# Optimization experiments

Hardware: AMD Instinct MI355X
Metric: run time of the kernel (lower is better)

## Reference

```python
import jax, jax.numpy as jnp
import numpy as np

NUM_CLASSES = 3
POS_T, NEG_T = 0.5, 0.3
RATIO = 3
W_OBJ, W_CLS, W_LOC = 1.0, 1.0, 2.0


def _pairwise_iou(a, b):
    # a: [N,4] anchors, b: [G,4] gt boxes, xyxy
    ix1 = jnp.maximum(a[:, None, 0], b[None, :, 0])
    iy1 = jnp.maximum(a[:, None, 1], b[None, :, 1])
    ix2 = jnp.minimum(a[:, None, 2], b[None, :, 2])
    iy2 = jnp.minimum(a[:, None, 3], b[None, :, 3])
    inter = jnp.clip(ix2 - ix1, 0) * jnp.clip(iy2 - iy1, 0)
    area_a = (a[:, 2] - a[:, 0]) * (a[:, 3] - a[:, 1])
    area_b = (b[:, 2] - b[:, 0]) * (b[:, 3] - b[:, 1])
    union = area_a[:, None] + area_b[None, :] - inter
    return inter / jnp.maximum(union, 1e-9)


def _masked_mean(x, m):
    c = m.sum()
    return jnp.where(c > 0, (x * m).sum() / jnp.maximum(c, 1.0), 0.0)


def _per_image(pred, anc, ax, ay, aw, ah, boxes_gt, labels_gt):
    # pred: [N, 5+nc]; anc: [N,4]; boxes_gt: [G,4]; labels_gt: [G] in 1..nc
    iou = _pairwise_iou(anc, boxes_gt)              # [N, G]
    best = jnp.argmax(iou, axis=1)
    best_iou = jnp.max(iou, axis=1)
    pos = best_iou >= POS_T
    neg = best_iou < NEG_T
    mb = boxes_gt[best]                             # matched boxes [N,4]
    ml = labels_gt[best]                            # matched labels [N]
    obj_logit = pred[:, 4]
    cls_logit = pred[:, 5:]
    obj_t = pos.astype(pred.dtype)
    # BCEWithLogits (numerically stable)
    obj_loss = jnp.maximum(obj_logit, 0) - obj_logit * obj_t + jnp.log1p(jnp.exp(-jnp.abs(obj_logit)))
    # hard negative mining: top-(3*num_pos) detached obj losses among negatives
    num_pos = pos.sum()
    k = jnp.minimum(RATIO * num_pos, neg.sum())
    cand = jnp.where(neg, jax.lax.stop_gradient(obj_loss), -1.0)
    order = jnp.argsort(-cand)
    ranks = jnp.zeros_like(order).at[order].set(jnp.arange(order.shape[0], dtype=order.dtype))
    sel_neg = neg & (ranks < k)
    loss_obj = _masked_mean(obj_loss, (pos | sel_neg).astype(pred.dtype))
    # classification over positives, labels shifted to 0-based
    logp = jax.nn.log_softmax(cls_logit, axis=-1)
    tgt = jnp.clip(ml - 1, 0)
    ce = -jnp.take_along_axis(logp, tgt[:, None], axis=1)[:, 0]
    loss_cls = _masked_mean(ce, pos.astype(pred.dtype))
    # localization over positives: SmoothL1 on encoded offsets
    gx = (mb[:, 0] + mb[:, 2]) * 0.5
    gy = (mb[:, 1] + mb[:, 3]) * 0.5
    gw = jnp.maximum(mb[:, 2] - mb[:, 0], 1e-6)
    gh = jnp.maximum(mb[:, 3] - mb[:, 1], 1e-6)
    loc_tgt = jnp.stack([(gx - ax) / aw, (gy - ay) / ah,
                         jnp.log(gw / aw), jnp.log(gh / ah)], axis=1)
    d = pred[:, :4] - loc_tgt
    ad = jnp.abs(d)
    sl1 = jnp.where(ad < 1.0, 0.5 * d * d, ad - 0.5)  # [N,4]
    pm = pos.astype(pred.dtype)
    cnt = 4.0 * pm.sum()
    loss_loc = jnp.where(cnt > 0, (sl1 * pm[:, None]).sum() / jnp.maximum(cnt, 1.0), 0.0)
    return loss_obj, loss_cls, loss_loc


def _detection_loss(preds, ancs, gt_boxes, gt_labels):
    B = preds[0].shape[0]
    obj_s = 0.0
    cls_s = 0.0
    loc_s = 0.0
    for pred, anc in zip(preds, ancs):
        Bp, C, H, W = pred.shape
        p = jnp.transpose(pred, (0, 2, 3, 1)).reshape(Bp, -1, 5 + NUM_CLASSES)
        ax = (anc[:, 0] + anc[:, 2]) * 0.5
        ay = (anc[:, 1] + anc[:, 3]) * 0.5
        aw = jnp.maximum(anc[:, 2] - anc[:, 0], 1e-6)
        ah = jnp.maximum(anc[:, 3] - anc[:, 1], 1e-6)
        lo, lc, ll = jax.vmap(
            lambda pb, bb, lb: _per_image(pb, anc, ax, ay, aw, ah, bb, lb)
        )(p, gt_boxes, gt_labels)
        obj_s = obj_s + lo.sum()
        cls_s = cls_s + lc.sum()
        loc_s = loc_s + ll.sum()
    obj_m = obj_s / B
    cls_m = cls_s / B
    loc_m = loc_s / B
    total = W_OBJ * obj_m + W_CLS * cls_m + W_LOC * loc_m
    return total, obj_m, cls_m, loc_m


def setup_inputs() -> dict:
    key = jax.random.key(0)
    k = jax.random.split(key, 8)
    B, G, A = 32, 50, 3
    img = 512.0
    scales = [(128, 128), (64, 64), (32, 32)]
    C = A * (5 + NUM_CLASSES)  # 24

    def make_anchors(H, W):
        stride = img / H
        ys, xs = np.meshgrid(np.arange(H), np.arange(W), indexing="ij")
        cx = (xs + 0.5) * stride
        cy = (ys + 0.5) * stride
        per = []
        for s in (1.0, 1.5, 2.0):
            half = s * stride
            per.append(np.stack([cx - half, cy - half, cx + half, cy + half], axis=-1).reshape(-1, 4))
        b = np.stack(per, axis=1).reshape(-1, 4)  # [H*W*A, 4], A innermost
        return jnp.asarray(b, dtype=jnp.float32)

    preds = [jax.random.normal(k[i], (B, C, H, W), dtype=jnp.float32) for i, (H, W) in enumerate(scales)]
    ancs = [make_anchors(H, W) for (H, W) in scales]
    cx = jax.random.uniform(k[3], (B, G)) * 384.0 + 64.0
    cy = jax.random.uniform(k[4], (B, G)) * 384.0 + 64.0
    w = jax.random.uniform(k[5], (B, G)) * 112.0 + 16.0
    h = jax.random.uniform(k[6], (B, G)) * 112.0 + 16.0
    gt_boxes = jnp.stack([cx - w / 2, cy - h / 2, cx + w / 2, cy + h / 2], axis=-1).astype(jnp.float32)
    gt_labels = jax.random.randint(k[7], (B, G), 1, NUM_CLASSES + 1)
    return {"p0": preds[0], "p1": preds[1], "p2": preds[2],
            "a0": ancs[0], "a1": ancs[1], "a2": ancs[2],
            "gt_boxes": gt_boxes, "gt_labels": gt_labels}


def reference(p0, p1, p2, a0, a1, a2, gt_boxes, gt_labels):
    return _detection_loss([p0, p1, p2], [a0, a1, a2], gt_boxes, gt_labels)
```

## Files before the change

kernel.cpp:

```cpp
#include <hip/hip_runtime.h>

#define WS_ACC_POS   0
#define WS_ACC_NEG   96
#define WS_ACC_OBJ   192
#define WS_ACC_CLS   288
#define WS_ACC_LOC   384
#define WS_SENT      480
#define WS_H1        512
#define WS_DONE      (512 + 96*192*2)
#define WS_TOTAL_U32 (WS_DONE + 96)

#define NBINS        192
#define BIN_OFF      872
#define SUM_SCALE    33554432.0f
#define INV_SUM_SCALE (1.0f/33554432.0f)

__device__ __forceinline__ float sl1f(float d){
  float ad = fabsf(d); return ad < 1.f ? 0.5f*d*d : ad - 0.5f;
}
__device__ __forceinline__ unsigned int rec_cnt(unsigned int v){
  return (v >= 0xA0000000u) ? (v - 0xAAAAAAAAu) : v;
}
__device__ __forceinline__ unsigned int ld_u32(unsigned int* p){
  return __hip_atomic_load(p, __ATOMIC_RELAXED, __HIP_MEMORY_SCOPE_AGENT);
}
__device__ __forceinline__ unsigned long long ld_u64(unsigned long long* p){
  return __hip_atomic_load(p, __ATOMIC_RELAXED, __HIP_MEMORY_SCOPE_AGENT);
}
__device__ __forceinline__ float ld_f32(float* p){
  return __hip_atomic_load(p, __ATOMIC_RELAXED, __HIP_MEMORY_SCOPE_AGENT);
}

__global__ __launch_bounds__(256) void k_main(
    const float* __restrict__ p0, const float* __restrict__ p1, const float* __restrict__ p2,
    const float* __restrict__ gtb, const int* __restrict__ gtl,
    unsigned int* __restrict__ ws, float* __restrict__ out)
{
  const int id = blockIdx.x;
  int s, bIm, chunk, H, lw; const float* p;
  if (id < 2048){ s=0; H=128; lw=7; chunk=id>>5;            bIm=id&31;          p=p0; }
  else if (id < 2560){ s=1; H=64; lw=6; chunk=(id-2048)>>5; bIm=(id-2048)&31;   p=p1; }
  else {              s=2; H=32; lw=5; chunk=(id-2560)>>5;  bIm=(id-2560)&31;   p=p2; }
  const int W = H, HW = H*W;
  const float stride = 512.0f/(float)H;
  const int g = s*32 + bIm;
  const int nb = (s==0) ? 64 : (s==1) ? 16 : 4;
  const int tid = threadIdx.x;

  __shared__ float4 sBox[52];
  __shared__ float  sArea[52], sGx[52], sGy[52], sGw[52], sGh[52];
  __shared__ int    sLbl[52];
  __shared__ int    sNk;
  __shared__ unsigned long long sH[NBINS];
  __shared__ float  sRF[3][4];
  __shared__ unsigned int sRU[4];
  __shared__ int    sLast;

  if (tid < 64){
    const int ymin = (chunk*256)>>lw;
    const int rowc = 256>>lw;
    const float by1 = ((float)ymin+0.5f)*stride - 2.0f*stride;
    const float by2 = ((float)(ymin+rowc-1)+0.5f)*stride + 2.0f*stride;
    bool keep=false; float4 gb=make_float4(0,0,0,0); int lbl=0;
    if (tid < 50){
      gb  = *(const float4*)(gtb + ((size_t)bIm*50 + tid)*4);
      lbl = gtl[bIm*50 + tid];
      keep = (fminf(by2, gb.w) - fmaxf(by1, gb.y)) > 0.f;
    }
    unsigned long long m = __ballot(keep);
    if (keep){
      int idx = __popcll(m & ((1ull<<tid)-1ull));
      sBox[idx]=gb;
      sArea[idx]=(gb.z-gb.x)*(gb.w-gb.y);
      sGx[idx]=(gb.x+gb.z)*0.5f;  sGy[idx]=(gb.y+gb.w)*0.5f;
      sGw[idx]=fmaxf(gb.z-gb.x,1e-6f); sGh[idx]=fmaxf(gb.w-gb.y,1e-6f);
      sLbl[idx]=lbl;
    }
    if (tid==0) sNk = __popcll(m);
  }
  if (tid < NBINS) sH[tid]=0ull;
  __syncthreads();

  const int nk = sNk;
  const int hw  = chunk*256 + tid;
  const int hwW = chunk*256 + (tid & ~63);
  const int y = hw>>lw, x = hw&(W-1);
  const float cx = ((float)x+0.5f)*stride, cy = ((float)y+0.5f)*stride;

  const float* pb = p + (size_t)bIm*24*HW + hw;
  float xo[3];
  #pragma unroll
  for (int a=0;a<3;a++) xo[a] = pb[(size_t)(a*8+4)*HW];

  const int wxlo = (W >= 64) ? (hwW & (W-1)) : 0;
  const int wxhi = (W >= 64) ? (wxlo + 63)   : (W-1);
  const int wylo = hwW>>lw, wyhi = (hwW+63)>>lw;
  const float m2 = 2.0f*stride;
  const float wx1 = ((float)wxlo+0.5f)*stride - m2;
  const float wx2 = ((float)wxhi+0.5f)*stride + m2;
  const float wy1 = ((float)wylo+0.5f)*stride - m2;
  const float wy2 = ((float)wyhi+0.5f)*stride + m2;

  float half[3]; half[0]=stride; half[1]=1.5f*stride; half[2]=2.0f*stride;
  float areaA[3], bi[3], bu[3]; int bj[3];
  #pragma unroll
  for (int a=0;a<3;a++){
    const float aw = 2.0f*half[a];
    areaA[a]=aw*aw; bi[a]=0.f; bu[a]=1e-9f; bj[a]=0;
  }
  for (int j=0;j<nk;j++){
    const float4 gb = sBox[j];
    if (gb.x >= wx2 || gb.z <= wx1 || gb.y >= wy2 || gb.w <= wy1) continue;
    const float ar = sArea[j];
    #pragma unroll
    for (int a=0;a<3;a++){
      const float iy1 = fmaxf(cy-half[a], gb.y), iy2 = fminf(cy+half[a], gb.w);
      const float ih  = fmaxf(iy2-iy1, 0.f);
      const float ix1 = fmaxf(cx-half[a], gb.x), ix2 = fminf(cx+half[a], gb.z);
      const float iw  = fmaxf(ix2-ix1, 0.f);
      const float inter = iw*ih;
      const float un = areaA[a] + ar - inter;
      if (inter*bu[a] > bi[a]*un){ bi[a]=inter; bu[a]=un; bj[a]=j; }
    }
  }

  int accPN=0;
  float accObj=0.f, accCls=0.f, accLoc=0.f;
  #pragma unroll
  for (int a=0;a<3;a++){
    const bool pos = bi[a] >= 0.5f*bu[a];
    const bool neg = bi[a] < 0.3f*bu[a];
    if (pos || neg){
      float objl = fmaxf(xo[a],0.f) - (pos ? xo[a] : 0.f)
                 + __logf(1.f + __expf(-fabsf(xo[a])));
      objl = fmaxf(objl, 0.f);
      if (neg){
        accPN += (1<<16);
        const int bin = min(max((int)(__float_as_uint(objl)>>20) - BIN_OFF, 0), NBINS-1);
        const unsigned long long pack =
            (1ull<<48) | (unsigned long long)__float2uint_rn(objl * SUM_SCALE);
        atomicAdd(&sH[bin], pack);
      } else {
        accPN += 1; accObj += objl;
        const int jb = bj[a];
        const float aw = 2.0f*half[a];
        const float c0=pb[(size_t)(a*8+5)*HW], c1=pb[(size_t)(a*8+6)*HW], c2=pb[(size_t)(a*8+7)*HW];
        const float mm = fmaxf(fmaxf(c0,c1),c2);
        const float lse = mm + __logf(__expf(c0-mm)+__expf(c1-mm)+__expf(c2-mm));
        const int t = max(sLbl[jb]-1, 0);
        const float ct = (t==0)?c0 : (t==1)?c1 : c2;
        accCls += lse - ct;
        const float tx = (sGx[jb]-cx)/aw;
        const float ty = (sGy[jb]-cy)/aw;
        const float tw = __logf(sGw[jb]/aw);
        const float th = __logf(sGh[jb]/aw);
        accLoc += sl1f(pb[(size_t)(a*8+0)*HW]-tx) + sl1f(pb[(size_t)(a*8+1)*HW]-ty)
                + sl1f(pb[(size_t)(a*8+2)*HW]-tw) + sl1f(pb[(size_t)(a*8+3)*HW]-th);
      }
    }
  }

  #pragma unroll
  for (int o=32;o;o>>=1){
    accPN  += __shfl_down(accPN,o,64);
    accObj += __shfl_down(accObj,o,64);
    accCls += __shfl_down(accCls,o,64);
    accLoc += __shfl_down(accLoc,o,64);
  }
  if ((tid & 63)==0){
    const int w = tid>>6;
    sRU[w]=(unsigned)accPN;
    sRF[0][w]=accObj; sRF[1][w]=accCls; sRF[2][w]=accLoc;
  }
  __syncthreads();
  if (tid==0){
    float* wf = (float*)ws;
    unsigned t=0; float ob=0,cl=0,lc=0;
    #pragma unroll
    for (int w=0;w<4;w++){ t+=sRU[w]; ob+=sRF[0][w]; cl+=sRF[1][w]; lc+=sRF[2][w]; }
    const unsigned pc = t & 0xFFFFu, nc = t >> 16;
    if (pc) atomicAdd(&ws[WS_ACC_POS+g], pc);
    if (nc) atomicAdd(&ws[WS_ACC_NEG+g], nc);
    if (ob!=0.f) atomicAdd(&wf[WS_ACC_OBJ+g], ob);
    if (cl!=0.f) atomicAdd(&wf[WS_ACC_CLS+g], cl);
    if (lc!=0.f) atomicAdd(&wf[WS_ACC_LOC+g], lc);
  }
  if (tid < NBINS){
    const unsigned long long v = sH[tid];
    if (v){
      unsigned long long* gH = (unsigned long long*)(ws + WS_H1) + (size_t)g*NBINS;
      atomicAdd(&gH[tid], v);
    }
  }

  __syncthreads();
  if (tid==0){
    __threadfence();
    const unsigned old = atomicAdd(&ws[WS_DONE+g], 1u);
    const unsigned b32 =
        (ld_u32(&ws[WS_SENT])==0xAAAAAAAAu) ? 0xAAAAAAAAu : 0u;
    sLast = ((old - b32) == (unsigned)(nb-1)) ? 1 : 0;
  }
  __syncthreads();
  if (!sLast || tid >= 64) return;

  __threadfence();
  const int lane = tid;
  float* wf = (float*)ws;
  const int pos  = (int)rec_cnt(ld_u32(&ws[WS_ACC_POS+g]));
  const int negc = (int)rec_cnt(ld_u32(&ws[WS_ACC_NEG+g]));
  const int k = min(3*pos, negc);
  float selSum = 0.f;

  if (k > 0){
    const unsigned long long base =
        (ld_u32(&ws[WS_SENT])==0xAAAAAAAAu) ? 0xAAAAAAAAAAAAAAAAull : 0ull;
    unsigned long long* gH = (unsigned long long*)(ws + WS_H1) + (size_t)g*NBINS;
    unsigned int c[3]; float sm[3];
    #pragma unroll
    for (int j=0;j<3;j++){
      const unsigned long long d = ld_u64(&gH[lane*3+j]) - base;
      c[j]  = (unsigned int)(d>>48);
      sm[j] = (float)(d & 0xFFFFFFFFFFFFull) * INV_SUM_SCALE;
    }
    const unsigned int c3 = c[0]+c[1]+c[2];
    unsigned int incl = c3;
    #pragma unroll
    for (int off=1; off<64; off<<=1){
      unsigned int yv = __shfl_down(incl, off, 64);
      if (lane+off < 64) incl += yv;
    }
    const unsigned int excl = incl - c3;
    int   tieL = -1, rL = 0; float avgL = 0.f;
    const bool hit = (excl < (unsigned)k) && (incl >= (unsigned)k);
    if (hit){
      unsigned int cum = excl;
      #pragma unroll
      for (int j=2;j>=0;j--){
        const unsigned int cc = c[j];
        if (cum + cc >= (unsigned)k){
          tieL = lane*3+j; rL = (int)((unsigned)k - cum);
          avgL = sm[j]/(float)cc;
          break;
        }
        cum += cc;
      }
    }
    const unsigned long long hm = __ballot(hit);
    const int src = __ffsll(hm) - 1;
    const int   tie = __shfl(tieL, src, 64);
    const int   r   = __shfl(rL,   src, 64);
    const float avg = __shfl(avgL, src, 64);
    float above = 0.f;
    #pragma unroll
    for (int j=0;j<3;j++) if (lane*3+j > tie) above += sm[j];
    #pragma unroll
    for (int o=32;o;o>>=1) above += __shfl_down(above,o,64);
    selSum = above + (float)r * avg;
  }
  if (lane==0){
    const int cObj = pos + k;
    const float ob = ld_f32(&wf[WS_ACC_OBJ+g]);
    const float cl = ld_f32(&wf[WS_ACC_CLS+g]);
    const float lcs= ld_f32(&wf[WS_ACC_LOC+g]);
    const float lo = (cObj>0) ? (ob+selSum)/(float)cObj : 0.f;
    const float lc = (pos>0)  ? cl/(float)pos           : 0.f;
    const float ll = (pos>0)  ? lcs/(float)(4*pos)      : 0.f;
    const float invB = 1.f/32.f;
    atomicAdd(out+0, (lo + lc + 2.f*ll)*invB);
    atomicAdd(out+1, lo*invB);
    atomicAdd(out+2, lc*invB);
    atomicAdd(out+3, ll*invB);
  }
}

extern "C" void kernel_launch(void* const* d_in, const int* in_sizes, int n_in,
                              void* d_out, int out_size, void* d_ws, size_t ws_size,
                              hipStream_t stream){
  if (ws_size < (size_t)WS_TOTAL_U32*4) return;
  const float* p0  = (const float*)d_in[0];
  const float* p1  = (const float*)d_in[1];
  const float* p2  = (const float*)d_in[2];
  const float* gtb = (const float*)d_in[6];
  const int*   gtl = (const int*)d_in[7];
  unsigned int* ws = (unsigned int*)d_ws;
  float* out = (float*)d_out;

  hipLaunchKernelGGL(k_main, dim3(2688), dim3(256), 0, stream,
                     p0,p1,p2,gtb,gtl,ws,out);
}
```

Measured before the change: 146.6 us.

## Replace atomic last-block reduction with per-block slots and second select kernel

Each block of the main kernel now writes its histogram and scalar partial sums into a private workspace slot instead of atomically accumulating into shared per-image counters and electing a last block through a done counter. A new 96-block kernel sums the slots per image and performs the hard-negative selection and final loss reduction. This removes global atomic contention, the sentinel-based workspace handling and the threadfence handshake, at the cost of an extra kernel launch and more workspace traffic (about 4 MB of slot writes and reads).

```diff
diff --git a/kernel.cpp b/kernel.cpp
--- a/kernel.cpp
+++ b/kernel.cpp
@@ -1,15 +1,7 @@
 #include <hip/hip_runtime.h>
 
-#define WS_ACC_POS   0
-#define WS_ACC_NEG   96
-#define WS_ACC_OBJ   192
-#define WS_ACC_CLS   288
-#define WS_ACC_LOC   384
-#define WS_SENT      480
-#define WS_H1        512
-#define WS_DONE      (512 + 96*192*2)
-#define WS_TOTAL_U32 (WS_DONE + 96)
-
+#define SLOT_U64     200
+#define NBLOCKS      2688
 #define NBINS        192
 #define BIN_OFF      872
 #define SUM_SCALE    33554432.0f
@@ -18,23 +10,11 @@
 __device__ __forceinline__ float sl1f(float d){
   float ad = fabsf(d); return ad < 1.f ? 0.5f*d*d : ad - 0.5f;
 }
-__device__ __forceinline__ unsigned int rec_cnt(unsigned int v){
-  return (v >= 0xA0000000u) ? (v - 0xAAAAAAAAu) : v;
-}
-__device__ __forceinline__ unsigned int ld_u32(unsigned int* p){
-  return __hip_atomic_load(p, __ATOMIC_RELAXED, __HIP_MEMORY_SCOPE_AGENT);
-}
-__device__ __forceinline__ unsigned long long ld_u64(unsigned long long* p){
-  return __hip_atomic_load(p, __ATOMIC_RELAXED, __HIP_MEMORY_SCOPE_AGENT);
-}
-__device__ __forceinline__ float ld_f32(float* p){
-  return __hip_atomic_load(p, __ATOMIC_RELAXED, __HIP_MEMORY_SCOPE_AGENT);
-}
 
 __global__ __launch_bounds__(256) void k_main(
     const float* __restrict__ p0, const float* __restrict__ p1, const float* __restrict__ p2,
     const float* __restrict__ gtb, const int* __restrict__ gtl,
-    unsigned int* __restrict__ ws, float* __restrict__ out)
+    unsigned long long* __restrict__ ws64)
 {
   const int id = blockIdx.x;
   int s, bIm, chunk, H, lw; const float* p;
@@ -43,8 +23,6 @@
   else {              s=2; H=32; lw=5; chunk=(id-2560)>>5;  bIm=(id-2560)&31;   p=p2; }
   const int W = H, HW = H*W;
   const float stride = 512.0f/(float)H;
-  const int g = s*32 + bIm;
-  const int nb = (s==0) ? 64 : (s==1) ? 16 : 4;
   const int tid = threadIdx.x;
 
   __shared__ float4 sBox[52];
@@ -54,7 +32,6 @@
   __shared__ unsigned long long sH[NBINS];
   __shared__ float  sRF[3][4];
   __shared__ unsigned int sRU[4];
-  __shared__ int    sLast;
 
   if (tid < 64){
     const int ymin = (chunk*256)>>lw;
@@ -173,53 +150,67 @@
     sRF[0][w]=accObj; sRF[1][w]=accCls; sRF[2][w]=accLoc;
   }
   __syncthreads();
+
+  unsigned long long* slot = ws64 + (size_t)id*SLOT_U64;
+  if (tid < NBINS) slot[tid] = sH[tid];
   if (tid==0){
-    float* wf = (float*)ws;
     unsigned t=0; float ob=0,cl=0,lc=0;
     #pragma unroll
     for (int w=0;w<4;w++){ t+=sRU[w]; ob+=sRF[0][w]; cl+=sRF[1][w]; lc+=sRF[2][w]; }
-    const unsigned pc = t & 0xFFFFu, nc = t >> 16;
-    if (pc) atomicAdd(&ws[WS_ACC_POS+g], pc);
-    if (nc) atomicAdd(&ws[WS_ACC_NEG+g], nc);
-    if (ob!=0.f) atomicAdd(&wf[WS_ACC_OBJ+g], ob);
-    if (cl!=0.f) atomicAdd(&wf[WS_ACC_CLS+g], cl);
-    if (lc!=0.f) atomicAdd(&wf[WS_ACC_LOC+g], lc);
-  }
+    slot[192] = ((unsigned long long)(t & 0xFFFFu) << 32) | (unsigned long long)(t >> 16);
+    slot[193] = (unsigned long long)__float_as_uint(ob);
+    slot[194] = (unsigned long long)__float_as_uint(cl);
+    slot[195] = (unsigned long long)__float_as_uint(lc);
+  }
+}
+
+__global__ __launch_bounds__(256) void k_select(const unsigned long long* __restrict__ ws64,
+                                                float* __restrict__ out){
+  const int g = blockIdx.x, tid = threadIdx.x;
+  const int s = g>>5, bIm = g&31;
+  const int nb   = (s==0)?64:(s==1)?16:4;
+  const int base = (s==0)?0:(s==1)?2048:2560;
+
+  __shared__ unsigned long long sHm[NBINS];
+  __shared__ unsigned int sPos, sNeg;
+  __shared__ float sObj, sCls, sLoc;
+
   if (tid < NBINS){
-    const unsigned long long v = sH[tid];
-    if (v){
-      unsigned long long* gH = (unsigned long long*)(ws + WS_H1) + (size_t)g*NBINS;
-      atomicAdd(&gH[tid], v);
-    }
-  }
-
+    unsigned long long a0=0ull, a1=0ull;
+    int b=0;
+    for (; b+1<nb; b+=2){
+      a0 += ws64[(size_t)(base + b*32 + bIm)*SLOT_U64 + tid];
+      a1 += ws64[(size_t)(base + (b+1)*32 + bIm)*SLOT_U64 + tid];
+    }
+    if (b<nb) a0 += ws64[(size_t)(base + b*32 + bIm)*SLOT_U64 + tid];
+    sHm[tid] = a0 + a1;
+  } else if (tid < 196){
+    const int j = tid - 192;
+    if (j==0){
+      unsigned long long t=0ull;
+      for (int b=0;b<nb;b++) t += ws64[(size_t)(base + b*32 + bIm)*SLOT_U64 + 192];
+      sPos = (unsigned)(t>>32); sNeg = (unsigned)(t & 0xFFFFFFFFull);
+    } else {
+      float f=0.f;
+      for (int b=0;b<nb;b++)
+        f += __uint_as_float((unsigned)ws64[(size_t)(base + b*32 + bIm)*SLOT_U64 + 192 + j]);
+      if (j==1) sObj=f; else if (j==2) sCls=f; else sLoc=f;
+    }
+  }
   __syncthreads();
-  if (tid==0){
-    __threadfence();
-    const unsigned old = atomicAdd(&ws[WS_DONE+g], 1u);
-    const unsigned b32 =
-        (ld_u32(&ws[WS_SENT])==0xAAAAAAAAu) ? 0xAAAAAAAAu : 0u;
-    sLast = ((old - b32) == (unsigned)(nb-1)) ? 1 : 0;
-  }
-  __syncthreads();
-  if (!sLast || tid >= 64) return;
-
-  __threadfence();
+  if (tid >= 64) return;
+
   const int lane = tid;
-  float* wf = (float*)ws;
-  const int pos  = (int)rec_cnt(ld_u32(&ws[WS_ACC_POS+g]));
-  const int negc = (int)rec_cnt(ld_u32(&ws[WS_ACC_NEG+g]));
+  const int pos  = (int)sPos;
+  const int negc = (int)sNeg;
   const int k = min(3*pos, negc);
   float selSum = 0.f;
 
   if (k > 0){
-    const unsigned long long base =
-        (ld_u32(&ws[WS_SENT])==0xAAAAAAAAu) ? 0xAAAAAAAAAAAAAAAAull : 0ull;
-    unsigned long long* gH = (unsigned long long*)(ws + WS_H1) + (size_t)g*NBINS;
     unsigned int c[3]; float sm[3];
     #pragma unroll
     for (int j=0;j<3;j++){
-      const unsigned long long d = ld_u64(&gH[lane*3+j]) - base;
+      const unsigned long long d = sHm[lane*3+j];
       c[j]  = (unsigned int)(d>>48);
       sm[j] = (float)(d & 0xFFFFFFFFFFFFull) * INV_SUM_SCALE;
     }
@@ -247,7 +238,7 @@
       }
     }
     const unsigned long long hm = __ballot(hit);
-    const int src = __ffsll(hm) - 1;
+    const int src = __ffsll((long long)hm) - 1;
     const int   tie = __shfl(tieL, src, 64);
     const int   r   = __shfl(rL,   src, 64);
     const float avg = __shfl(avgL, src, 64);
@@ -260,12 +251,9 @@
   }
   if (lane==0){
     const int cObj = pos + k;
-    const float ob = ld_f32(&wf[WS_ACC_OBJ+g]);
-    const float cl = ld_f32(&wf[WS_ACC_CLS+g]);
-    const float lcs= ld_f32(&wf[WS_ACC_LOC+g]);
-    const float lo = (cObj>0) ? (ob+selSum)/(float)cObj : 0.f;
-    const float lc = (pos>0)  ? cl/(float)pos           : 0.f;
-    const float ll = (pos>0)  ? lcs/(float)(4*pos)      : 0.f;
+    const float lo = (cObj>0) ? (sObj+selSum)/(float)cObj : 0.f;
+    const float lc = (pos>0)  ? sCls/(float)pos           : 0.f;
+    const float ll = (pos>0)  ? sLoc/(float)(4*pos)       : 0.f;
     const float invB = 1.f/32.f;
     atomicAdd(out+0, (lo + lc + 2.f*ll)*invB);
     atomicAdd(out+1, lo*invB);
@@ -277,15 +265,15 @@
 extern "C" void kernel_launch(void* const* d_in, const int* in_sizes, int n_in,
                               void* d_out, int out_size, void* d_ws, size_t ws_size,
                               hipStream_t stream){
-  if (ws_size < (size_t)WS_TOTAL_U32*4) return;
+  if (ws_size < (size_t)NBLOCKS*SLOT_U64*8) return;
   const float* p0  = (const float*)d_in[0];
   const float* p1  = (const float*)d_in[1];
   const float* p2  = (const float*)d_in[2];
   const float* gtb = (const float*)d_in[6];
   const int*   gtl = (const int*)d_in[7];
-  unsigned int* ws = (unsigned int*)d_ws;
+  unsigned long long* ws64 = (unsigned long long*)d_ws;
   float* out = (float*)d_out;
 
-  hipLaunchKernelGGL(k_main, dim3(2688), dim3(256), 0, stream,
-                     p0,p1,p2,gtb,gtl,ws,out);
-}
+  hipLaunchKernelGGL(k_main,   dim3(NBLOCKS), dim3(256), 0, stream, p0,p1,p2,gtb,gtl,ws64);
+  hipLaunchKernelGGL(k_select, dim3(96),      dim3(256), 0, stream, ws64, out);
+}
```

Measured after the change: 141.2 us. 1.04x faster.
